# Kernel tuning notes

Hardware: AMD Instinct MI355X
Metric: run time of the kernel (lower is better)

## Reference

```python
import jax, jax.numpy as jnp
import numpy as np

MAX_REL = 14
HEADS = 12
HEAD_DIM = 64
SCALE = HEAD_DIM ** -0.5


def _rel_indices(length):
    # Replicates ElasticRelativePosition2D index construction (static, numpy).
    L = length - 1
    s = int(L ** 0.5)
    r = np.arange(L)
    dv = r[None, :] // s - r[:, None] // s
    dh = r[None, :] % s - r[:, None] % s
    iv = np.clip(dv, -MAX_REL, MAX_REL) + MAX_REL + 1
    ih = np.clip(dh, -MAX_REL, MAX_REL) + MAX_REL + 1
    # pad top row and left col with index 0 (the CLS slot)
    iv = np.pad(iv, ((1, 0), (1, 0)), constant_values=0)
    ih = np.pad(ih, ((1, 0), (1, 0)), constant_values=0)
    return jnp.asarray(iv, dtype=jnp.int32), jnp.asarray(ih, dtype=jnp.int32)


def _rel_emb(table_v, table_h, length):
    iv, ih = _rel_indices(length)
    return table_v[iv] + table_h[ih]  # [length, length, 64]


def setup_inputs() -> dict:
    key = jax.random.key(0)
    ks = jax.random.split(key, 16)
    B, L, D = 32, 577, 768
    T = 2 * MAX_REL + 2  # 30
    std = 0.02
    inp = {
        "q": jax.random.normal(ks[0], (B, L, D), jnp.float32),
        "k": jax.random.normal(ks[1], (B, L, D), jnp.float32),
        "v": jax.random.normal(ks[2], (B, L, D), jnp.float32),
        "Wq": jax.random.normal(ks[3], (D, HEADS * HEAD_DIM), jnp.float32) * std,
        "bq": jnp.zeros((HEADS * HEAD_DIM,), jnp.float32),
        "Wk": jax.random.normal(ks[4], (D, HEADS * HEAD_DIM), jnp.float32) * std,
        "bk": jnp.zeros((HEADS * HEAD_DIM,), jnp.float32),
        "Wv": jax.random.normal(ks[5], (D, HEADS * HEAD_DIM), jnp.float32) * std,
        "bv": jnp.zeros((HEADS * HEAD_DIM,), jnp.float32),
        "Wp": jax.random.normal(ks[6], (HEADS * HEAD_DIM, D), jnp.float32) * std,
        "bp": jnp.zeros((D,), jnp.float32),
        "tab_vk": jax.random.normal(ks[7], (T, HEAD_DIM), jnp.float32) * std,
        "tab_hk": jax.random.normal(ks[8], (T, HEAD_DIM), jnp.float32) * std,
        "tab_vv": jax.random.normal(ks[9], (T, HEAD_DIM), jnp.float32) * std,
        "tab_hv": jax.random.normal(ks[10], (T, HEAD_DIM), jnp.float32) * std,
    }
    return inp


def reference(q, k, v, Wq, bq, Wk, bk, Wv, bv, Wp, bp, tab_vk, tab_hk, tab_vv, tab_hv):
    B, L, D = q.shape
    residual = q
    qh = (q @ Wq + bq).reshape(B, L, HEADS, HEAD_DIM).transpose(0, 2, 1, 3)  # [B,H,L,d]
    kh = (k @ Wk + bk).reshape(B, L, HEADS, HEAD_DIM).transpose(0, 2, 1, 3)
    vh = (v @ Wv + bv).reshape(B, L, HEADS, HEAD_DIM).transpose(0, 2, 1, 3)

    attn = jnp.einsum("bhid,bhjd->bhij", qh, kh) * SCALE
    r_p_k = _rel_emb(tab_vk, tab_hk, L)  # [L,L,d]
    attn = attn + jnp.einsum("bhid,ijd->bhij", qh, r_p_k)  # bias NOT scaled (as in source)
    attn = jax.nn.softmax(attn, axis=-1)

    out = jnp.einsum("bhij,bhjd->bhid", attn, vh)
    r_p_v = _rel_emb(tab_vv, tab_hv, L)
    out = out + jnp.einsum("bhij,ijd->bhid", attn, r_p_v)
    out = out.transpose(0, 2, 1, 3).reshape(B, L, HEADS * HEAD_DIM)

    out = out @ Wp + bp
    return out + residual
```

## Files before the change

kernel.cpp:

```cpp
#include <hip/hip_runtime.h>
#include <cstdint>


typedef unsigned short u16;
typedef unsigned int   u32;
typedef __attribute__((ext_vector_type(8))) __bf16 bf16x8;
typedef __attribute__((ext_vector_type(4))) float  f32x4;

#define B_   32
#define L_   577
#define D_   768
#define H_   12
#define HD_  64
#define LP_  640
#define M_   (B_*L_)
#define SCALE_ 0.125f

__device__ __forceinline__ float b2f(u16 u){ u32 x = ((u32)u) << 16; float f; __builtin_memcpy(&f,&x,4); return f; }
__device__ __forceinline__ u16 f2b(float f){ u32 x; __builtin_memcpy(&x,&f,4); u32 r = (x + 0x7FFFu + ((x>>16)&1u)) >> 16; return (u16)r; }

__device__ __forceinline__ f32x4 mfma_bf16(bf16x8 a, bf16x8 b, f32x4 c){
  return __builtin_amdgcn_mfma_f32_16x16x32_bf16(a, b, c, 0, 0, 0);
}

__device__ __forceinline__ void async16(const void* g, void* l){
  __builtin_amdgcn_global_load_lds(
    (const __attribute__((address_space(1))) void*)g,
    (__attribute__((address_space(3))) void*)l,
    16, 0, 0);
}

__device__ __forceinline__ void lds_fence(){
  asm volatile("s_waitcnt lgkmcnt(0)" ::: "memory");
}
__device__ __forceinline__ void cbar(){
  asm volatile("" ::: "memory");
}

__global__ __launch_bounds__(256) void ind_setup(u16* __restrict__ ind)
{
  int jt = blockIdx.x;
  int t  = threadIdx.x;
  int nt = t >> 6, lane = t & 63;
  int qq = lane >> 4, cc = lane & 15;
  int n = nt*16 + cc;
  u16 vals[8];
  #pragma unroll
  for (int idx = 0; idx < 8; ++idx){
    int j = jt*32 + qq*8 + idx;
    int bv, bhh;
    if (j == 0){ bv = 24; bhh = 24; }
    else { int jj = j-1; bv = jj/24; if (bv > 23) bv = 23; bhh = jj - (jj/24)*24; }
    bool one = (n < 25) ? (bv == n) : ((n < 50) ? (bhh == n-25) : false);
    vals[idx] = one ? (u16)0x3F80 : (u16)0;
  }
  *(uint4*)&ind[(size_t)((jt*4 + nt)*64 + lane)*8] = *(uint4*)vals;
}

__global__ __launch_bounds__(256) void tab_setup(
    const float* __restrict__ tvk, const float* __restrict__ thk,
    const float* __restrict__ tvv, const float* __restrict__ thv,
    u16* __restrict__ tabK, u16* __restrict__ tabVT)
{
  int i = blockIdx.x*256 + threadIdx.x;
  if (i >= 64*64) return;
  int r = i >> 6, col = i & 63;
  float kv = 0.f;
  if (r < 30)      kv = tvk[r*HD_ + col];
  else if (r < 60) kv = thk[(r-30)*HD_ + col];
  tabK[i] = f2b(kv);
  float vv = 0.f;
  if (col < 30)      vv = tvv[col*HD_ + r];
  else if (col < 60) vv = thv[(col-30)*HD_ + r];
  tabVT[i] = f2b(vv);
}

__global__ __launch_bounds__(256) void cvt3_bf16(
    const float* __restrict__ q, const float* __restrict__ k, const float* __restrict__ v,
    u16* __restrict__ dq, u16* __restrict__ dk, u16* __restrict__ dv)
{
  int z = blockIdx.y;
  const float* s = (z==0)?q:(z==1)?k:v;
  u16*         d = (z==0)?dq:(z==1)?dk:dv;
  int i = blockIdx.x*256 + threadIdx.x;
  if (i >= (M_*D_)/8) return;
  const float4* s4 = (const float4*)s;
  float4 a = s4[2*i], b = s4[2*i+1];
  uint4 o;
  o.x = (u32)f2b(a.x) | ((u32)f2b(a.y)<<16);
  o.y = (u32)f2b(a.z) | ((u32)f2b(a.w)<<16);
  o.z = (u32)f2b(b.x) | ((u32)f2b(b.y)<<16);
  o.w = (u32)f2b(b.z) | ((u32)f2b(b.w)<<16);
  ((uint4*)d)[i] = o;
}

__global__ __launch_bounds__(256) void transpose768(
    const float* __restrict__ W0, const float* __restrict__ W1,
    const float* __restrict__ W2, const float* __restrict__ W3,
    u16* __restrict__ T0, u16* __restrict__ T1, u16* __restrict__ T2, u16* __restrict__ T3)
{
  __shared__ float t[32][33];
  int z = blockIdx.z;
  const float* W = (z==0)?W0:(z==1)?W1:(z==2)?W2:W3;
  u16*         T = (z==0)?T0:(z==1)?T1:(z==2)?T2:T3;
  int kb = blockIdx.x*32, nb = blockIdx.y*32;
  int tx = threadIdx.x & 31, ty = threadIdx.x >> 5;
  #pragma unroll
  for (int r=0;r<32;r+=8) t[ty+r][tx] = W[(size_t)(kb+ty+r)*768 + nb+tx];
  __syncthreads();
  #pragma unroll
  for (int r=0;r<32;r+=8) T[(size_t)(nb+ty+r)*768 + kb+tx] = f2b(t[tx][ty+r]);
}

__global__ __launch_bounds__(256) void vtr_kernel(
    const u16* __restrict__ vh, u16* __restrict__ vhT)
{
  __shared__ __align__(16) u16 t[64][72];
  int ll0 = blockIdx.x * 64;
  size_t bhs = (size_t)(blockIdx.z*H_ + blockIdx.y) * LP_ * HD_;
  const u16* src = vh + bhs;
  u16* dst = vhT + bhs;
  int tid = threadIdx.x;
  #pragma unroll
  for (int it=0; it<2; ++it){
    int idx = it*256 + tid;
    int row = idx >> 3, ch = (idx & 7)*8;
    uint4 d4; d4.x=0u; d4.y=0u; d4.z=0u; d4.w=0u;
    if (ll0 + row < L_) d4 = *(const uint4*)(src + (size_t)(ll0+row)*HD_ + ch);
    *(uint4*)&t[row][ch] = d4;
  }
  __syncthreads();
  #pragma unroll
  for (int it=0; it<2; ++it){
    int idx = it*256 + tid;
    int dd = idx >> 3, l8 = (idx & 7)*8;
    u16 vals[8];
    #pragma unroll
    for (int e=0;e<8;++e) vals[e] = t[l8+e][dd];
    *(uint4*)(dst + (size_t)dd*LP_ + ll0 + l8) = *(uint4*)vals;
  }
}

__global__ __launch_bounds__(256) void gemm_qkv(
    const u16* __restrict__ Aq, const u16* __restrict__ Ak, const u16* __restrict__ Av,
    const u16* __restrict__ WTbase,
    const float* __restrict__ bq, const float* __restrict__ bk, const float* __restrict__ bv,
    u16* __restrict__ Dq, u16* __restrict__ Dk, u16* __restrict__ Dv)
{
  __shared__ __align__(16) u16 AsL[128*32];
  __shared__ __align__(16) u16 BsL[128*32];
  const int blk = blockIdx.x;
  const int which = blk / 912;
  const int inner = blk - which*912;
  const int x = inner & 7, g = inner >> 3;
  const int n0 = (g % 6) * 128;
  const int m_idx = (g / 6) * 8 + x;
  if (m_idx >= 145) return;
  const int m0 = m_idx * 128;

  const u16* A  = (which==0)?Aq:(which==1)?Ak:Av;
  const u16* BT = WTbase + (size_t)which*768*768;
  const float* bias = (which==0)?bq:(which==1)?bk:bv;
  u16* Dst = (which==0)?Dq:(which==1)?Dk:Dv;

  const int tid = threadIdx.x;
  const int w = tid>>6, lane = tid&63, q = lane>>4, c = lane&15;
  const int wr = w>>1, wc = w&1;

  f32x4 acc[4][4];
  #pragma unroll
  for (int ai=0;ai<4;++ai)
    #pragma unroll
    for (int bi=0;bi<4;++bi){ f32x4 z = {0.f,0.f,0.f,0.f}; acc[ai][bi] = z; }

  for (int k0 = 0; k0 < 768; k0 += 32){
    __syncthreads();
    #pragma unroll
    for (int t2 = 0; t2 < 2; ++t2){
      int idx = t2*256 + tid;
      int row = idx >> 2, ch = idx & 3;
      int mrow = m0 + row; if (mrow > M_-1) mrow = M_-1;
      async16(A + (size_t)mrow*768 + k0 + ch*8, (char*)AsL + (size_t)(t2*256 + w*64)*16);
      async16(BT + (size_t)(n0 + row)*768 + k0 + ch*8, (char*)BsL + (size_t)(t2*256 + w*64)*16);
    }
    __syncthreads();

    bf16x8 af[4], bf2[4];
    #pragma unroll
    for (int ai=0;ai<4;++ai) af[ai]  = *(const bf16x8*)&AsL[(wr*64 + ai*16 + c)*32 + q*8];
    #pragma unroll
    for (int bi=0;bi<4;++bi) bf2[bi] = *(const bf16x8*)&BsL[(wc*64 + bi*16 + c)*32 + q*8];
    #pragma unroll
    for (int ai=0;ai<4;++ai)
      #pragma unroll
      for (int bi=0;bi<4;++bi)
        acc[ai][bi] = mfma_bf16(af[ai], bf2[bi], acc[ai][bi]);
  }

  #pragma unroll
  for (int ai=0;ai<4;++ai){
    #pragma unroll
    for (int r2=0;r2<4;++r2){
      int mrow = m0 + wr*64 + ai*16 + q*4 + r2;
      if (mrow >= M_) continue;
      int bb = mrow / L_;
      int ll = mrow - bb*L_;
      #pragma unroll
      for (int bi=0;bi<4;++bi){
        int col = n0 + wc*64 + bi*16 + c;
        float vv = acc[ai][bi][r2] + bias[col];
        int hh = col >> 6, dd = col & 63;
        Dst[(((size_t)(bb*H_ + hh)*LP_ + ll) << 6) + dd] = f2b(vv);
      }
    }
  }
}

__global__ __launch_bounds__(256) void gemm_kernel(
    const u16* __restrict__ A, const u16* __restrict__ BT,
    const float* __restrict__ bias, const float* __restrict__ resid,
    void* __restrict__ Dstv, int mode)
{
  __shared__ __align__(16) u16 AsL[128*32];
  __shared__ __align__(16) u16 BsL[128*32];
  const int blk = blockIdx.x;
  const int x = blk & 7, g = blk >> 3;
  const int n0 = (g % 6) * 128;
  const int m_idx = (g / 6) * 8 + x;
  if (m_idx >= 145) return;
  const int m0 = m_idx * 128;

  const int tid = threadIdx.x;
  const int w = tid>>6, lane = tid&63, q = lane>>4, c = lane&15;
  const int wr = w>>1, wc = w&1;

  f32x4 acc[4][4];
  #pragma unroll
  for (int ai=0;ai<4;++ai)
    #pragma unroll
    for (int bi=0;bi<4;++bi){ f32x4 z = {0.f,0.f,0.f,0.f}; acc[ai][bi] = z; }

  for (int k0 = 0; k0 < 768; k0 += 32){
    __syncthreads();
    #pragma unroll
    for (int t2 = 0; t2 < 2; ++t2){
      int idx = t2*256 + tid;
      int row = idx >> 2, ch = idx & 3;
      int mrow = m0 + row; if (mrow > M_-1) mrow = M_-1;
      const u16* srcA;
      if (mode < 3) srcA = A + (size_t)mrow*768 + k0 + ch*8;
      else {
        int bb = mrow / L_, ll = mrow - bb*L_;
        int hh = k0 >> 6, dd = (k0 & 63) + ch*8;
        srcA = A + (((size_t)(bb*H_ + hh)*LP_ + ll) << 6) + dd;
      }
      async16(srcA, (char*)AsL + (size_t)(t2*256 + w*64)*16);
      async16(BT + (size_t)(n0 + row)*768 + k0 + ch*8, (char*)BsL + (size_t)(t2*256 + w*64)*16);
    }
    __syncthreads();

    bf16x8 af[4], bf2[4];
    #pragma unroll
    for (int ai=0;ai<4;++ai) af[ai]  = *(const bf16x8*)&AsL[(wr*64 + ai*16 + c)*32 + q*8];
    #pragma unroll
    for (int bi=0;bi<4;++bi) bf2[bi] = *(const bf16x8*)&BsL[(wc*64 + bi*16 + c)*32 + q*8];
    #pragma unroll
    for (int ai=0;ai<4;++ai)
      #pragma unroll
      for (int bi=0;bi<4;++bi)
        acc[ai][bi] = mfma_bf16(af[ai], bf2[bi], acc[ai][bi]);
  }

  #pragma unroll
  for (int ai=0;ai<4;++ai){
    #pragma unroll
    for (int r2=0;r2<4;++r2){
      int mrow = m0 + wr*64 + ai*16 + q*4 + r2;
      if (mrow >= M_) continue;
      int bb = mrow / L_;
      int ll = mrow - bb*L_;
      #pragma unroll
      for (int bi=0;bi<4;++bi){
        int col = n0 + wc*64 + bi*16 + c;
        float vv = acc[ai][bi][r2] + bias[col];
        if (mode < 3){
          int hh = col >> 6, dd = col & 63;
          ((u16*)Dstv)[(((size_t)(bb*H_ + hh)*LP_ + ll) << 6) + dd] = f2b(vv);
        } else {
          size_t o2 = (size_t)mrow*768 + col;
          ((float*)Dstv)[o2] = vv + resid[o2];
        }
      }
    }
  }
}

__global__ __launch_bounds__(256) void attn_kernel(
    const u16* __restrict__ qh, const u16* __restrict__ kh, const u16* __restrict__ vhT,
    const u16* __restrict__ tabK, const u16* __restrict__ tabVT,
    const u16* __restrict__ ind,
    u16* __restrict__ oh)
{
  __shared__ __align__(16) char sb[4*5632];
  const int tid = threadIdx.x;
  const int w = tid>>6, lane = tid&63, q = lane>>4, c = lane&15;
  char* wb = sb + w*5632;
  u16*   pvhb  = (u16*)wb;
  u16*   Ps0   = (u16*)wb;
  u16*   Ps1   = (u16*)(wb + 1280);
  float* gvh   = (float*)wb;
  u16*   bias_t= (u16*)(wb + 3328);
  u16*   Wm    = (u16*)(wb + 3328);

  const int id = blockIdx.x;
  const int lin = (id & 7)*480 + (id >> 3);
  const int qt = lin % 10;
  const int hb = lin / 10;
  const int h = hb % 12, b = hb / 12;

  const int i0 = qt * 64;
  const size_t bh = (size_t)(b*H_ + h) * LP_ * HD_;
  const u16* qh_b = qh + bh;
  const u16* kh_b = kh + bh;
  const u16* vT_b = vhT + bh;

  bf16x8 aq0 = *(const bf16x8*)(qh_b + (size_t)(i0 + w*16 + c)*HD_ + q*8);
  bf16x8 aq1 = *(const bf16x8*)(qh_b + (size_t)(i0 + w*16 + c)*HD_ + 32 + q*8);

  #pragma unroll
  for (int nt=0; nt<4; ++nt){
    bf16x8 tb0 = *(const bf16x8*)(tabK + (size_t)(nt*16+c)*64 + q*8);
    bf16x8 tb1 = *(const bf16x8*)(tabK + (size_t)(nt*16+c)*64 + 32 + q*8);
    f32x4 s = {0.f,0.f,0.f,0.f};
    s = mfma_bf16(aq0, tb0, s);
    s = mfma_bf16(aq1, tb1, s);
    int bin = nt*16 + c;
    if (bin < 60){
      #pragma unroll
      for (int r=0;r<4;++r) pvhb[(q*4+r)*66 + bin] = f2b(s[r]);
    }
  }
  lds_fence();

  for (int o = lane; o < 16*50; o += 64){
    int row = o / 50, t = o - (o/50)*50;
    int ig = i0 + w*16 + row;
    const u16* src = pvhb + row*66;
    u16 val;
    if (ig == 0){
      val = src[t < 25 ? 0 : 30];
    } else {
      int im1 = ig - 1;
      int rr = im1 / 24, cc2 = im1 - (im1/24)*24;
      if (t < 25){
        if (t == 24) val = src[0];
        else { int d = t - rr;  d = d < -14 ? -14 : (d > 14 ? 14 : d); val = src[15 + d]; }
      } else {
        int cb = t - 25;
        if (cb == 24) val = src[30];
        else { int d = cb - cc2; d = d < -14 ? -14 : (d > 14 ? 14 : d); val = src[45 + d]; }
      }
    }
    bias_t[row*52 + t] = val;
  }
  lds_fence();

  int ig_[4];
  #pragma unroll
  for (int r=0;r<4;++r) ig_[r] = i0 + w*16 + q*4 + r;

  const u16* btr = bias_t + (q*4)*52;

  auto qk_softmax = [&](int jtx, u16* dst){
    int j0x = jtx * 32;
    #pragma unroll
    for (int sub=0; sub<2; ++sub){
      const u16* kr = kh_b + (size_t)(j0x + sub*16 + c)*HD_;
      bf16x8 bk0 = *(const bf16x8*)(kr + q*8);
      bf16x8 bk1 = *(const bf16x8*)(kr + 32 + q*8);
      f32x4 s4 = {0.f,0.f,0.f,0.f};
      __builtin_amdgcn_s_setprio(1);
      s4 = mfma_bf16(aq0, bk0, s4);
      s4 = mfma_bf16(aq1, bk1, s4);
      __builtin_amdgcn_s_setprio(0);

      int j  = j0x + sub*16 + c;
      bool jv = (j < L_);
      int jj = j - 1;
      int q24 = jj / 24;
      int gR  = (j==0) ? 24 : (q24 > 23 ? 23 : q24);
      int cbR = (j==0) ? 24 : (jj - q24*24);

      #pragma unroll
      for (int r=0;r<4;++r){
        float bias = b2f(btr[r*52 + gR]) + b2f(btr[r*52 + 25 + cbR]);
        float s = fmaf(s4[r], SCALE_, bias);
        s = fminf(fmaxf(s, -80.f), 30.f);
        float p = jv ? __expf(s) : 0.f;
        __bf16 pb = (__bf16)p;
        u16 pu; __builtin_memcpy(&pu, &pb, 2);
        dst[(q*4+r)*40 + sub*16 + c] = pu;
      }
    }
  };

  f32x4 o4[4], hist[4];
  #pragma unroll
  for (int nt=0;nt<4;++nt){ f32x4 z = {0.f,0.f,0.f,0.f}; o4[nt] = z; hist[nt] = z; }

  qk_softmax(0, Ps0);

  for (int jt = 0; jt < 19; ++jt){
    int j0 = jt * 32;
    bf16x8 bvf[4];
    #pragma unroll
    for (int nt=0;nt<4;++nt)
      bvf[nt] = *(const bf16x8*)(vT_b + (size_t)(nt*16+c)*LP_ + j0 + q*8);
    uint4 bi_raw[4];
    #pragma unroll
    for (int nt=0;nt<4;++nt) bi_raw[nt] = ((const uint4*)ind)[(jt*4 + nt)*64 + lane];

    cbar();
    u16* Pc = (jt & 1) ? Ps1 : Ps0;
    bf16x8 ap = *(const bf16x8*)(Pc + c*40 + q*8);

    if (jt < 18) qk_softmax(jt+1, (jt & 1) ? Ps0 : Ps1);

    __builtin_amdgcn_s_setprio(1);
    #pragma unroll
    for (int nt=0;nt<4;++nt){
      o4[nt] = mfma_bf16(ap, bvf[nt], o4[nt]);
      bf16x8 bI = *(const bf16x8*)&bi_raw[nt];
      hist[nt] = mfma_bf16(ap, bI, hist[nt]);
    }
    __builtin_amdgcn_s_setprio(0);
  }

  lds_fence();

  #pragma unroll
  for (int nt=0;nt<4;++nt){
    int bin = nt*16 + c;
    if (bin < 50){
      #pragma unroll
      for (int r=0;r<4;++r)
        gvh[(size_t)(q*4 + r)*52 + bin] = hist[nt][r];
    }
  }
  lds_fence();

  for (int o = lane; o < 16*72; o += 64) Wm[o] = 0;
  lds_fence();
  if (lane < 16){
    int ig = i0 + w*16 + lane;
    const float* gv = gvh + (size_t)lane*52;
    u16* wrp = Wm + lane*72;
    if (ig == 0){
      float sv=0.f, sh=0.f;
      for (int g2=0; g2<25; ++g2){ sv += gv[g2]; sh += gv[25+g2]; }
      wrp[0] = f2b(sv); wrp[30] = f2b(sh);
    } else {
      int rr = (ig-1)/24, cc2 = (ig-1) - ((ig-1)/24)*24;
      wrp[0]  = f2b(gv[24]);
      wrp[30] = f2b(gv[49]);
      for (int t=1; t<30; ++t){
        float sv = 0.f, sh = 0.f;
        if (t == 1){
          for (int g2=0; g2 <= rr-14  && g2 < 24; ++g2) sv += gv[g2];
          for (int c2=0; c2 <= cc2-14 && c2 < 24; ++c2) sh += gv[25+c2];
        } else if (t == 29){
          for (int g2 = (rr+14  < 0 ? 0 : rr+14 ); g2 < 24; ++g2) sv += gv[g2];
          for (int c2 = (cc2+14 < 0 ? 0 : cc2+14); c2 < 24; ++c2) sh += gv[25+c2];
        } else {
          int g2 = rr  + t - 15; if (g2 >= 0 && g2 < 24) sv = gv[g2];
          int c2 = cc2 + t - 15; if (c2 >= 0 && c2 < 24) sh = gv[25+c2];
        }
        wrp[t] = f2b(sv); wrp[30+t] = f2b(sh);
      }
    }
  }
  lds_fence();

  bf16x8 aw0 = *(const bf16x8*)(Wm + c*72 + q*8);
  bf16x8 aw1 = *(const bf16x8*)(Wm + c*72 + 32 + q*8);
  __builtin_amdgcn_s_setprio(1);
  #pragma unroll
  for (int nt=0;nt<4;++nt){
    bf16x8 bt0 = *(const bf16x8*)(tabVT + (size_t)(nt*16+c)*64 + q*8);
    bf16x8 bt1 = *(const bf16x8*)(tabVT + (size_t)(nt*16+c)*64 + 32 + q*8);
    o4[nt] = mfma_bf16(aw0, bt0, o4[nt]);
    o4[nt] = mfma_bf16(aw1, bt1, o4[nt]);
  }
  __builtin_amdgcn_s_setprio(0);

  u16* oh_b = oh + bh;
  #pragma unroll
  for (int r=0;r<4;++r){
    if (ig_[r] < L_){
      const float* gr = gvh + (size_t)(q*4 + r)*52;
      f32x4 a0 = *(const f32x4*)(gr);
      f32x4 a1 = *(const f32x4*)(gr+4);
      f32x4 a2 = *(const f32x4*)(gr+8);
      f32x4 a3 = *(const f32x4*)(gr+12);
      f32x4 a4 = *(const f32x4*)(gr+16);
      f32x4 a5 = *(const f32x4*)(gr+20);
      float lsum = (a0[0]+a0[1]+a0[2]+a0[3]) + (a1[0]+a1[1]+a1[2]+a1[3])
                 + (a2[0]+a2[1]+a2[2]+a2[3]) + (a3[0]+a3[1]+a3[2]+a3[3])
                 + (a4[0]+a4[1]+a4[2]+a4[3]) + (a5[0]+a5[1]+a5[2]+a5[3]) + gr[24];
      float inv = 1.f / lsum;
      #pragma unroll
      for (int nt=0;nt<4;++nt)
        oh_b[(size_t)ig_[r]*HD_ + nt*16 + c] = f2b(o4[nt][r] * inv);
    }
  }
}

extern "C" void kernel_launch(void* const* d_in, const int* in_sizes, int n_in,
                              void* d_out, int out_size, void* d_ws, size_t ws_size,
                              hipStream_t stream)
{
  (void)in_sizes; (void)n_in; (void)out_size; (void)ws_size;
  const float* q_   = (const float*)d_in[0];
  const float* k_   = (const float*)d_in[1];
  const float* v_   = (const float*)d_in[2];
  const float* Wq_  = (const float*)d_in[3];
  const float* bq_  = (const float*)d_in[4];
  const float* Wk_  = (const float*)d_in[5];
  const float* bk_  = (const float*)d_in[6];
  const float* Wv_  = (const float*)d_in[7];
  const float* bv_  = (const float*)d_in[8];
  const float* Wp_  = (const float*)d_in[9];
  const float* bp_  = (const float*)d_in[10];
  const float* tvk_ = (const float*)d_in[11];
  const float* thk_ = (const float*)d_in[12];
  const float* tvv_ = (const float*)d_in[13];
  const float* thv_ = (const float*)d_in[14];

  char* ws = (char*)d_ws;
  const size_t szHead = (size_t)B_*H_*LP_*HD_*2;
  const size_t szQKV  = (size_t)M_*D_*2;
  u16* qh   = (u16*)(ws);
  u16* kh   = (u16*)(ws + szHead);
  u16* vh   = (u16*)(ws + 2*szHead);
  u16* oh   = (u16*)(ws + 3*szHead);
  u16* q_bf = oh;
  u16* k_bf = (u16*)(ws + 4*szHead);
  u16* v_bf = (u16*)(ws + 4*szHead + szQKV);
  u16* vhT  = k_bf;
  u16* WqT  = (u16*)(ws + 4*szHead + 2*szQKV);
  u16* WkT  = WqT + 768*768;
  u16* WvT  = WkT + 768*768;
  u16* WpT  = WvT + 768*768;
  u16* ind  = WpT + 768*768;
  u16* tabK  = ind + 19*4*64*8;
  u16* tabVT = tabK + 64*64;

  ind_setup<<<19, 256, 0, stream>>>(ind);
  tab_setup<<<16, 256, 0, stream>>>(tvk_, thk_, tvv_, thv_, tabK, tabVT);
  transpose768<<<dim3(24,24,4), 256, 0, stream>>>(Wq_, Wk_, Wv_, Wp_, WqT, WkT, WvT, WpT);
  cvt3_bf16<<<dim3((M_*D_/8 + 255)/256, 3), 256, 0, stream>>>(q_, k_, v_, q_bf, k_bf, v_bf);
  gemm_qkv<<<2736, 256, 0, stream>>>(q_bf, k_bf, v_bf, WqT, bq_, bk_, bv_, qh, kh, vh);
  vtr_kernel<<<dim3(10,12,32), 256, 0, stream>>>(vh, vhT);
  attn_kernel<<<3840, 256, 0, stream>>>(qh, kh, vhT, tabK, tabVT, ind, oh);
  gemm_kernel<<<912, 256, 0, stream>>>(oh, WpT, bp_, q_, d_out, 3);
}
```

Baseline: 792.5 us.

## Prefetch K fragments two tiles ahead in attention loop and merge setup kernels

Inside the attention kernel, the K-tile fragments used by the QK^T MFMAs are now loaded into registers two iterations ahead and rotated through a double buffer. This hides global-load latency behind the PV MFMAs and softmax work. The two small setup kernels are also merged into one launch to save launch overhead. The cost is more live VGPRs, which could lower occupancy, plus an added lgkmcnt wait in the loop.

Measured after the change: 784.5 us. No clear change (-1.0%).

```diff
diff --git a/kernel.cpp b/kernel.cpp
--- a/kernel.cpp
+++ b/kernel.cpp
@@ -37,42 +37,42 @@
   asm volatile("" ::: "memory");
 }
 
-__global__ __launch_bounds__(256) void ind_setup(u16* __restrict__ ind)
-{
-  int jt = blockIdx.x;
-  int t  = threadIdx.x;
-  int nt = t >> 6, lane = t & 63;
-  int qq = lane >> 4, cc = lane & 15;
-  int n = nt*16 + cc;
-  u16 vals[8];
-  #pragma unroll
-  for (int idx = 0; idx < 8; ++idx){
-    int j = jt*32 + qq*8 + idx;
-    int bv, bhh;
-    if (j == 0){ bv = 24; bhh = 24; }
-    else { int jj = j-1; bv = jj/24; if (bv > 23) bv = 23; bhh = jj - (jj/24)*24; }
-    bool one = (n < 25) ? (bv == n) : ((n < 50) ? (bhh == n-25) : false);
-    vals[idx] = one ? (u16)0x3F80 : (u16)0;
-  }
-  *(uint4*)&ind[(size_t)((jt*4 + nt)*64 + lane)*8] = *(uint4*)vals;
-}
-
-__global__ __launch_bounds__(256) void tab_setup(
+__global__ __launch_bounds__(256) void setup_kernel(
     const float* __restrict__ tvk, const float* __restrict__ thk,
     const float* __restrict__ tvv, const float* __restrict__ thv,
-    u16* __restrict__ tabK, u16* __restrict__ tabVT)
-{
-  int i = blockIdx.x*256 + threadIdx.x;
-  if (i >= 64*64) return;
-  int r = i >> 6, col = i & 63;
-  float kv = 0.f;
-  if (r < 30)      kv = tvk[r*HD_ + col];
-  else if (r < 60) kv = thk[(r-30)*HD_ + col];
-  tabK[i] = f2b(kv);
-  float vv = 0.f;
-  if (col < 30)      vv = tvv[col*HD_ + r];
-  else if (col < 60) vv = thv[(col-30)*HD_ + r];
-  tabVT[i] = f2b(vv);
+    u16* __restrict__ ind, u16* __restrict__ tabK, u16* __restrict__ tabVT)
+{
+  int bx = blockIdx.x;
+  if (bx < 19){
+    int jt = bx;
+    int t  = threadIdx.x;
+    int nt = t >> 6, lane = t & 63;
+    int qq = lane >> 4, cc = lane & 15;
+    int n = nt*16 + cc;
+    u16 vals[8];
+    #pragma unroll
+    for (int idx = 0; idx < 8; ++idx){
+      int j = jt*32 + qq*8 + idx;
+      int bv, bhh;
+      if (j == 0){ bv = 24; bhh = 24; }
+      else { int jj = j-1; bv = jj/24; if (bv > 23) bv = 23; bhh = jj - (jj/24)*24; }
+      bool one = (n < 25) ? (bv == n) : ((n < 50) ? (bhh == n-25) : false);
+      vals[idx] = one ? (u16)0x3F80 : (u16)0;
+    }
+    *(uint4*)&ind[(size_t)((jt*4 + nt)*64 + lane)*8] = *(uint4*)vals;
+  } else {
+    int i = (bx-19)*256 + threadIdx.x;
+    if (i >= 64*64) return;
+    int r = i >> 6, col = i & 63;
+    float kv = 0.f;
+    if (r < 30)      kv = tvk[r*HD_ + col];
+    else if (r < 60) kv = thk[(r-30)*HD_ + col];
+    tabK[i] = f2b(kv);
+    float vv = 0.f;
+    if (col < 30)      vv = tvv[col*HD_ + r];
+    else if (col < 60) vv = thv[(col-30)*HD_ + r];
+    tabVT[i] = f2b(vv);
+  }
 }
 
 __global__ __launch_bounds__(256) void cvt3_bf16(
@@ -371,17 +371,23 @@
 
   const u16* btr = bias_t + (q*4)*52;
 
-  auto qk_softmax = [&](int jtx, u16* dst){
+  auto load_kf = [&](int jtx, bf16x8* kf){
+    const u16* kr0 = kh_b + (size_t)(jtx*32 + c)*HD_;
+    const u16* kr1 = kh_b + (size_t)(jtx*32 + 16 + c)*HD_;
+    kf[0] = *(const bf16x8*)(kr0 + q*8);
+    kf[1] = *(const bf16x8*)(kr0 + 32 + q*8);
+    kf[2] = *(const bf16x8*)(kr1 + q*8);
+    kf[3] = *(const bf16x8*)(kr1 + 32 + q*8);
+  };
+
+  auto qk_softmax = [&](int jtx, const bf16x8* kf, u16* dst){
     int j0x = jtx * 32;
     #pragma unroll
     for (int sub=0; sub<2; ++sub){
-      const u16* kr = kh_b + (size_t)(j0x + sub*16 + c)*HD_;
-      bf16x8 bk0 = *(const bf16x8*)(kr + q*8);
-      bf16x8 bk1 = *(const bf16x8*)(kr + 32 + q*8);
       f32x4 s4 = {0.f,0.f,0.f,0.f};
       __builtin_amdgcn_s_setprio(1);
-      s4 = mfma_bf16(aq0, bk0, s4);
-      s4 = mfma_bf16(aq1, bk1, s4);
+      s4 = mfma_bf16(aq0, kf[2*sub], s4);
+      s4 = mfma_bf16(aq1, kf[2*sub+1], s4);
       __builtin_amdgcn_s_setprio(0);
 
       int j  = j0x + sub*16 + c;
@@ -408,7 +414,10 @@
   #pragma unroll
   for (int nt=0;nt<4;++nt){ f32x4 z = {0.f,0.f,0.f,0.f}; o4[nt] = z; hist[nt] = z; }
 
-  qk_softmax(0, Ps0);
+  bf16x8 kf_cur[4], kf_nxt[4];
+  load_kf(0, kf_cur);
+  qk_softmax(0, kf_cur, Ps0);
+  load_kf(1, kf_cur);
 
   for (int jt = 0; jt < 19; ++jt){
     int j0 = jt * 32;
@@ -419,12 +428,14 @@
     uint4 bi_raw[4];
     #pragma unroll
     for (int nt=0;nt<4;++nt) bi_raw[nt] = ((const uint4*)ind)[(jt*4 + nt)*64 + lane];
+    if (jt < 17) load_kf(jt+2, kf_nxt);
 
     cbar();
     u16* Pc = (jt & 1) ? Ps1 : Ps0;
     bf16x8 ap = *(const bf16x8*)(Pc + c*40 + q*8);
-
-    if (jt < 18) qk_softmax(jt+1, (jt & 1) ? Ps0 : Ps1);
+    lds_fence();
+
+    if (jt < 18) qk_softmax(jt+1, kf_cur, (jt & 1) ? Ps0 : Ps1);
 
     __builtin_amdgcn_s_setprio(1);
     #pragma unroll
@@ -434,6 +445,9 @@
       hist[nt] = mfma_bf16(ap, bI, hist[nt]);
     }
     __builtin_amdgcn_s_setprio(0);
+
+    #pragma unroll
+    for (int e=0;e<4;++e) kf_cur[e] = kf_nxt[e];
   }
 
   lds_fence();
@@ -555,8 +569,7 @@
   u16* tabK  = ind + 19*4*64*8;
   u16* tabVT = tabK + 64*64;
 
-  ind_setup<<<19, 256, 0, stream>>>(ind);
-  tab_setup<<<16, 256, 0, stream>>>(tvk_, thk_, tvv_, thv_, tabK, tabVT);
+  setup_kernel<<<35, 256, 0, stream>>>(tvk_, thk_, tvv_, thv_, ind, tabK, tabVT);
   transpose768<<<dim3(24,24,4), 256, 0, stream>>>(Wq_, Wk_, Wv_, Wp_, WqT, WkT, WvT, WpT);
   cvt3_bf16<<<dim3((M_*D_/8 + 255)/256, 3), 256, 0, stream>>>(q_, k_, v_, q_bf, k_bf, v_bf);
   gemm_qkv<<<2736, 256, 0, stream>>>(q_bf, k_bf, v_bf, WqT, bq_, bk_, bv_, qh, kh, vh);
```
